# Performance work log

Hardware: AMD Instinct MI355X
Metric: run time of the kernel (lower is better)

## Reference

```python
import jax, jax.numpy as jnp
import numpy as np
from jax import lax

# quantization bit widths (config)
IB, WB, RB, AB = 8, 4, 4, 8


def quantize(x, bw):
    """Signed fixed-point quantization to bw bits in [-1, 1) with STE."""
    scale = 2.0 ** (bw - 1)
    q = jnp.clip(jnp.round(x * scale), -scale, scale - 1) / scale
    return x + lax.stop_gradient(q - x)


def setup_inputs() -> dict:
    key = jax.random.key(0)
    k1, k2, k3, k4, k5 = jax.random.split(key, 5)
    B, T, I, H, O = 256, 1024, 64, 256, 16
    inputs = jax.random.normal(k1, (B, T, I), dtype=jnp.float32)
    # input kernel init: uniform(-1, 1)
    Wi = jax.random.uniform(k2, (H, I), dtype=jnp.float32, minval=-1.0, maxval=1.0)
    # recurrent kernel: orthogonal (geotorch parametrization); materialize via QR
    A = jax.random.normal(k3, (H, H), dtype=jnp.float32)
    Wr, _ = jnp.linalg.qr(A)
    Wr = Wr.astype(jnp.float32)
    Wo = jax.random.normal(k4, (O, H), dtype=jnp.float32) * 0.1
    b = jax.random.normal(k5, (H,), dtype=jnp.float32) * 0.01
    return {"inputs": inputs, "Wi": Wi, "Wr": Wr, "Wo": Wo, "b": b}


def reference(inputs, Wi, Wr, Wo, b):
    # quantize inputs (ib bits)
    x = quantize(inputs, IB)
    # quantized input projection, precomputed for all timesteps: [B,T,H]
    u = jnp.einsum("bti,hi->bth", x, quantize(Wi, WB))
    Wrq = quantize(Wr, RB)  # quantized orthogonal recurrent weight [H,H]
    B = inputs.shape[0]
    H = Wr.shape[0]
    h0 = jnp.zeros((B, H), dtype=inputs.dtype)

    def step(h, u_t):
        z = u_t + h @ Wrq.T                      # [B,H]
        m = jax.nn.relu(jnp.abs(z) + b)          # modrelu magnitude
        h_new = quantize(jnp.sign(z) * m, AB)    # quantized activation
        return h_new, None

    u_t = jnp.swapaxes(u, 0, 1)  # [T,B,H]
    h_last, _ = lax.scan(step, h0, u_t)
    # output head on last hidden state
    out = h_last @ quantize(Wo, WB).T  # [B,O]
    return out
```

## Files before the change

### kernel.cpp

```cpp
#include <hip/hip_runtime.h>


#define TSEQ 1024
#define IDIM 64
#define HDIM 256
#define ODIM 16

__device__ __forceinline__ int sdot4i8(int a, int b, int c) {
#if __has_builtin(__builtin_amdgcn_sdot4)
    return __builtin_amdgcn_sdot4(a, b, c, false);
#else
    int r = c;
    r += ((a << 24) >> 24) * ((b << 24) >> 24);
    r += ((a << 16) >> 24) * ((b << 16) >> 24);
    r += ((a << 8)  >> 24) * ((b << 8)  >> 24);
    r += (a >> 24) * (b >> 24);
    return r;
#endif
}

__device__ __forceinline__ int qpack4(float4 f, float s, float lo, float hi) {
    int a = (int)fminf(fmaxf(rintf(f.x * s), lo), hi);
    int b = (int)fminf(fmaxf(rintf(f.y * s), lo), hi);
    int c = (int)fminf(fmaxf(rintf(f.z * s), lo), hi);
    int d = (int)fminf(fmaxf(rintf(f.w * s), lo), hi);
    return (a & 255) | ((b & 255) << 8) | ((c & 255) << 16) | ((d & 255) << 24);
}

__device__ __forceinline__ int qsum(int v) {
    v += __builtin_amdgcn_update_dpp(0, v, 0xB1, 0xF, 0xF, true);
    v += __builtin_amdgcn_update_dpp(0, v, 0x4E, 0xF, 0xF, true);
    return v;
}

__global__ __launch_bounds__(256, 1)
void qornn_kernel(const float* __restrict__ x, const float* __restrict__ Wi,
                  const float* __restrict__ Wr, const float* __restrict__ Wo,
                  const float* __restrict__ bias, float* __restrict__ out) {
    __shared__ alignas(16) int xlds[TSEQ * 16 + 16];
    __shared__ alignas(16) int wstage[8192];
    __shared__ alignas(16) int hbuf[2][64];

    const int tid = threadIdx.x;
    const int brow = blockIdx.x;
    const int w    = tid >> 6;
    const int l    = tid & 63;
    const int q    = l & 3;
    const int m16  = l >> 2;
    const int obase = w * 64 + m16 * 4;

    {
        const float4* wi4 = (const float4*)Wi;
        #pragma unroll
        for (int it = 0; it < 16; ++it) {
            int flat = it * 256 + tid;
            wstage[flat] = qpack4(wi4[flat], 8.0f, -8.0f, 7.0f);
        }
    }
    __syncthreads();
    int4 wiq[4];
    {
        const int4* p = (const int4*)wstage;
        #pragma unroll
        for (int i = 0; i < 4; ++i) wiq[i] = p[(obase + i) * 4 + q];
    }
    __syncthreads();

    int4 wr[16];
    {
        const float4* wr4 = (const float4*)Wr;
        #pragma unroll
        for (int it = 0; it < 32; ++it) {
            int flat = it * 256 + tid;
            wstage[flat] = qpack4(wr4[flat], 8.0f, -8.0f, 7.0f);
        }
        __syncthreads();
        if (obase < 128) {
            const int4* p = (const int4*)wstage;
            #pragma unroll
            for (int i = 0; i < 4; ++i)
                #pragma unroll
                for (int r = 0; r < 4; ++r)
                    wr[i * 4 + r] = p[(obase + i) * 16 + q * 4 + r];
        }
        __syncthreads();
        #pragma unroll
        for (int it = 0; it < 32; ++it) {
            int flat = it * 256 + tid;
            wstage[flat] = qpack4(wr4[8192 + flat], 8.0f, -8.0f, 7.0f);
        }
        __syncthreads();
        if (obase >= 128) {
            const int4* p = (const int4*)wstage;
            #pragma unroll
            for (int i = 0; i < 4; ++i)
                #pragma unroll
                for (int r = 0; r < 4; ++r)
                    wr[i * 4 + r] = p[(obase - 128 + i) * 16 + q * 4 + r];
        }
        __syncthreads();
    }

    {
        const float4* wo4 = (const float4*)Wo;
        #pragma unroll
        for (int it = 0; it < 4; ++it) {
            int flat = it * 256 + tid;
            wstage[flat] = qpack4(wo4[flat], 8.0f, -8.0f, 7.0f);
        }
    }

    {
        const float4* rowf4 = (const float4*)(x + (size_t)brow * (TSEQ * IDIM));
        #pragma unroll 8
        for (int it = 0; it < 64; ++it) {
            int flat = it * 256 + tid;
            xlds[flat] = qpack4(rowf4[flat], 128.0f, -128.0f, 127.0f);
        }
    }
    if (tid < 64) hbuf[0][tid] = 0;
    __syncthreads();

    const float bv = bias[tid];
    const bool qb0 = (q & 1) != 0;
    const bool qb1 = (q & 2) != 0;

    int u[4];
    {
        const int4 xx = ((const int4*)xlds)[q];
        #pragma unroll
        for (int i = 0; i < 4; ++i) {
            int s = sdot4i8(xx.x, wiq[i].x, 0);
            s = sdot4i8(xx.y, wiq[i].y, s);
            s = sdot4i8(xx.z, wiq[i].z, s);
            u[i] = sdot4i8(xx.w, wiq[i].w, s);
        }
    }

    #pragma unroll 2
    for (int t = 0; t < TSEQ; ++t) {
        int4 hh[4];
        {
            const int4* hP = (const int4*)hbuf[t & 1];
            #pragma unroll
            for (int r = 0; r < 4; ++r) hh[r] = hP[q * 4 + r];
        }
        const int4 xn = ((const int4*)xlds)[(t + 1) * 4 + q];

        int za[4], zb[4];
        #pragma unroll
        for (int i = 0; i < 4; ++i) {
            int s0 = u[i];
            s0 = sdot4i8(hh[0].x, wr[i * 4 + 0].x, s0);
            s0 = sdot4i8(hh[0].y, wr[i * 4 + 0].y, s0);
            s0 = sdot4i8(hh[0].z, wr[i * 4 + 0].z, s0);
            s0 = sdot4i8(hh[0].w, wr[i * 4 + 0].w, s0);
            s0 = sdot4i8(hh[1].x, wr[i * 4 + 1].x, s0);
            s0 = sdot4i8(hh[1].y, wr[i * 4 + 1].y, s0);
            s0 = sdot4i8(hh[1].z, wr[i * 4 + 1].z, s0);
            s0 = sdot4i8(hh[1].w, wr[i * 4 + 1].w, s0);
            int s1 = 0;
            s1 = sdot4i8(hh[2].x, wr[i * 4 + 2].x, s1);
            s1 = sdot4i8(hh[2].y, wr[i * 4 + 2].y, s1);
            s1 = sdot4i8(hh[2].z, wr[i * 4 + 2].z, s1);
            s1 = sdot4i8(hh[2].w, wr[i * 4 + 2].w, s1);
            s1 = sdot4i8(hh[3].x, wr[i * 4 + 3].x, s1);
            s1 = sdot4i8(hh[3].y, wr[i * 4 + 3].y, s1);
            s1 = sdot4i8(hh[3].z, wr[i * 4 + 3].z, s1);
            s1 = sdot4i8(hh[3].w, wr[i * 4 + 3].w, s1);
            za[i] = s0; zb[i] = s1;
        }
        int un[4];
        #pragma unroll
        for (int i = 0; i < 4; ++i) {
            int s = sdot4i8(xn.x, wiq[i].x, 0);
            s = sdot4i8(xn.y, wiq[i].y, s);
            s = sdot4i8(xn.z, wiq[i].z, s);
            un[i] = sdot4i8(xn.w, wiq[i].w, s);
        }

        const int z0 = qsum(za[0] + zb[0]);
        const int z1 = qsum(za[1] + zb[1]);
        const int z2 = qsum(za[2] + zb[2]);
        const int z3 = qsum(za[3] + zb[3]);
        const int zlo = qb0 ? z1 : z0;
        const int zhi = qb0 ? z3 : z2;
        const int z   = qb1 ? zhi : zlo;

        const float zf = (float)z;
        const float t1 = fmaf(fabsf(zf), 0.0009765625f, bv);
        const float t2 = fmaxf(t1, 0.0f);
        const float r  = rintf(t2 * 128.0f);
        const int vpos = (int)fminf(r, 127.0f);
        const int vneg = -(int)fminf(r, 128.0f);
        int hv = (z < 0) ? vneg : vpos;
        hv = (z == 0) ? 0 : hv;

        ((signed char*)hbuf[(t + 1) & 1])[tid] = (signed char)hv;

        #pragma unroll
        for (int i = 0; i < 4; ++i) u[i] = un[i];
        __syncthreads();
    }

    if (tid < ODIM) {
        const int4* wo = (const int4*)wstage;
        const int4* hl = (const int4*)hbuf[0];
        int a0 = 0, a1 = 0, a2 = 0, a3 = 0;
        #pragma unroll
        for (int i = 0; i < 16; ++i) {
            int4 w4 = wo[tid * 16 + i];
            int4 h4 = hl[i];
            a0 = sdot4i8(h4.x, w4.x, a0);
            a1 = sdot4i8(h4.y, w4.y, a1);
            a2 = sdot4i8(h4.z, w4.z, a2);
            a3 = sdot4i8(h4.w, w4.w, a3);
        }
        out[brow * ODIM + tid] = (float)((a0 + a1) + (a2 + a3)) * 0.0009765625f;
    }
}

extern "C" void kernel_launch(void* const* d_in, const int* in_sizes, int n_in,
                              void* d_out, int out_size, void* d_ws, size_t ws_size,
                              hipStream_t stream) {
    const float* x  = (const float*)d_in[0];
    const float* Wi = (const float*)d_in[1];
    const float* Wr = (const float*)d_in[2];
    const float* Wo = (const float*)d_in[3];
    const float* b  = (const float*)d_in[4];
    float* out = (float*)d_out;

    const int B = in_sizes[0] / (TSEQ * IDIM);
    qornn_kernel<<<B, HDIM, 0, stream>>>(x, Wi, Wr, Wo, b, out);
}
```

Baseline: 422.1 us.

## Compute recurrent matvec with int8 MFMA instead of per-lane sdot4 and DPP reduction

The per-step recurrent product h·Wrᵀ now runs on 16x16x64 int8 MFMA instructions, with the quantized Wr held in registers in A-operand layout and the hidden state read as the B operand. Each lane then picks its own output element out of the accumulator tile. This replaces 64 sdot4 instructions and a DPP cross-lane reduction per lane. The input projection is reorganised so each lane computes one full dot product for its output row. The B operand's 16 columns are all the same hidden vector, so most of the MFMA work is redundant. The cost being attacked is per-step instruction latency on the serial critical path.

```diff
diff --git a/kernel.cpp b/kernel.cpp
--- a/kernel.cpp
+++ b/kernel.cpp
@@ -5,6 +5,8 @@
 #define IDIM 64
 #define HDIM 256
 #define ODIM 16
+
+using i32x4 = __attribute__((ext_vector_type(4))) int;
 
 __device__ __forceinline__ int sdot4i8(int a, int b, int c) {
 #if __has_builtin(__builtin_amdgcn_sdot4)
@@ -27,12 +29,6 @@
     return (a & 255) | ((b & 255) << 8) | ((c & 255) << 16) | ((d & 255) << 24);
 }
 
-__device__ __forceinline__ int qsum(int v) {
-    v += __builtin_amdgcn_update_dpp(0, v, 0xB1, 0xF, 0xF, true);
-    v += __builtin_amdgcn_update_dpp(0, v, 0x4E, 0xF, 0xF, true);
-    return v;
-}
-
 __global__ __launch_bounds__(256, 1)
 void qornn_kernel(const float* __restrict__ x, const float* __restrict__ Wi,
                   const float* __restrict__ Wr, const float* __restrict__ Wo,
@@ -43,11 +39,12 @@
 
     const int tid = threadIdx.x;
     const int brow = blockIdx.x;
-    const int w    = tid >> 6;
-    const int l    = tid & 63;
-    const int q    = l & 3;
-    const int m16  = l >> 2;
-    const int obase = w * 64 + m16 * 4;
+    const int w   = tid >> 6;
+    const int l   = tid & 63;
+    const int lm  = l & 15;
+    const int lg  = l >> 4;
+    const int olocal = ((l & 15) >> 2) * 16 + lg * 4 + (l & 3);
+    const int oglob  = w * 64 + olocal;
 
     {
         const float4* wi4 = (const float4*)Wi;
@@ -58,15 +55,15 @@
         }
     }
     __syncthreads();
-    int4 wiq[4];
+    int4 wi[4];
     {
         const int4* p = (const int4*)wstage;
         #pragma unroll
-        for (int i = 0; i < 4; ++i) wiq[i] = p[(obase + i) * 4 + q];
+        for (int i = 0; i < 4; ++i) wi[i] = p[oglob * 4 + i];
     }
     __syncthreads();
 
-    int4 wr[16];
+    i32x4 wrA[4][4];
     {
         const float4* wr4 = (const float4*)Wr;
         #pragma unroll
@@ -75,13 +72,13 @@
             wstage[flat] = qpack4(wr4[flat], 8.0f, -8.0f, 7.0f);
         }
         __syncthreads();
-        if (obase < 128) {
-            const int4* p = (const int4*)wstage;
+        if (w < 2) {
+            const i32x4* p = (const i32x4*)wstage;
             #pragma unroll
-            for (int i = 0; i < 4; ++i)
+            for (int tt = 0; tt < 4; ++tt)
                 #pragma unroll
-                for (int r = 0; r < 4; ++r)
-                    wr[i * 4 + r] = p[(obase + i) * 16 + q * 4 + r];
+                for (int s = 0; s < 4; ++s)
+                    wrA[tt][s] = p[(w * 64 + tt * 16 + lm) * 16 + s * 4 + lg];
         }
         __syncthreads();
         #pragma unroll
@@ -90,13 +87,13 @@
             wstage[flat] = qpack4(wr4[8192 + flat], 8.0f, -8.0f, 7.0f);
         }
         __syncthreads();
-        if (obase >= 128) {
-            const int4* p = (const int4*)wstage;
+        if (w >= 2) {
+            const i32x4* p = (const i32x4*)wstage;
             #pragma unroll
-            for (int i = 0; i < 4; ++i)
+            for (int tt = 0; tt < 4; ++tt)
                 #pragma unroll
-                for (int r = 0; r < 4; ++r)
-                    wr[i * 4 + r] = p[(obase - 128 + i) * 16 + q * 4 + r];
+                for (int s = 0; s < 4; ++s)
+                    wrA[tt][s] = p[((w - 2) * 64 + tt * 16 + lm) * 16 + s * 4 + lg];
         }
         __syncthreads();
     }
@@ -121,71 +118,60 @@
     if (tid < 64) hbuf[0][tid] = 0;
     __syncthreads();
 
-    const float bv = bias[tid];
-    const bool qb0 = (q & 1) != 0;
-    const bool qb1 = (q & 2) != 0;
-
-    int u[4];
-    {
-        const int4 xx = ((const int4*)xlds)[q];
-        #pragma unroll
-        for (int i = 0; i < 4; ++i) {
-            int s = sdot4i8(xx.x, wiq[i].x, 0);
-            s = sdot4i8(xx.y, wiq[i].y, s);
-            s = sdot4i8(xx.z, wiq[i].z, s);
-            u[i] = sdot4i8(xx.w, wiq[i].w, s);
-        }
-    }
+    const float bv = bias[oglob];
+    const bool tb1 = (l & 8) != 0;
+    const bool tb0 = (l & 4) != 0;
+    const bool rb1 = (l & 2) != 0;
+    const bool rb0 = (l & 1) != 0;
+
+    int u = 0;
+    #pragma unroll
+    for (int s = 0; s < 4; ++s) {
+        const int4 xx = ((const int4*)xlds)[s];
+        u = sdot4i8(xx.x, wi[s].x, u);
+        u = sdot4i8(xx.y, wi[s].y, u);
+        u = sdot4i8(xx.z, wi[s].z, u);
+        u = sdot4i8(xx.w, wi[s].w, u);
+    }
+
+    const i32x4 zero4 = {0, 0, 0, 0};
 
     #pragma unroll 2
     for (int t = 0; t < TSEQ; ++t) {
-        int4 hh[4];
+        i32x4 hB[4];
         {
-            const int4* hP = (const int4*)hbuf[t & 1];
+            const i32x4* hP = (const i32x4*)hbuf[t & 1];
             #pragma unroll
-            for (int r = 0; r < 4; ++r) hh[r] = hP[q * 4 + r];
-        }
-        const int4 xn = ((const int4*)xlds)[(t + 1) * 4 + q];
-
-        int za[4], zb[4];
-        #pragma unroll
-        for (int i = 0; i < 4; ++i) {
-            int s0 = u[i];
-            s0 = sdot4i8(hh[0].x, wr[i * 4 + 0].x, s0);
-            s0 = sdot4i8(hh[0].y, wr[i * 4 + 0].y, s0);
-            s0 = sdot4i8(hh[0].z, wr[i * 4 + 0].z, s0);
-            s0 = sdot4i8(hh[0].w, wr[i * 4 + 0].w, s0);
-            s0 = sdot4i8(hh[1].x, wr[i * 4 + 1].x, s0);
-            s0 = sdot4i8(hh[1].y, wr[i * 4 + 1].y, s0);
-            s0 = sdot4i8(hh[1].z, wr[i * 4 + 1].z, s0);
-            s0 = sdot4i8(hh[1].w, wr[i * 4 + 1].w, s0);
-            int s1 = 0;
-            s1 = sdot4i8(hh[2].x, wr[i * 4 + 2].x, s1);
-            s1 = sdot4i8(hh[2].y, wr[i * 4 + 2].y, s1);
-            s1 = sdot4i8(hh[2].z, wr[i * 4 + 2].z, s1);
-            s1 = sdot4i8(hh[2].w, wr[i * 4 + 2].w, s1);
-            s1 = sdot4i8(hh[3].x, wr[i * 4 + 3].x, s1);
-            s1 = sdot4i8(hh[3].y, wr[i * 4 + 3].y, s1);
-            s1 = sdot4i8(hh[3].z, wr[i * 4 + 3].z, s1);
-            s1 = sdot4i8(hh[3].w, wr[i * 4 + 3].w, s1);
-            za[i] = s0; zb[i] = s1;
-        }
-        int un[4];
-        #pragma unroll
-        for (int i = 0; i < 4; ++i) {
-            int s = sdot4i8(xn.x, wiq[i].x, 0);
-            s = sdot4i8(xn.y, wiq[i].y, s);
-            s = sdot4i8(xn.z, wiq[i].z, s);
-            un[i] = sdot4i8(xn.w, wiq[i].w, s);
-        }
-
-        const int z0 = qsum(za[0] + zb[0]);
-        const int z1 = qsum(za[1] + zb[1]);
-        const int z2 = qsum(za[2] + zb[2]);
-        const int z3 = qsum(za[3] + zb[3]);
-        const int zlo = qb0 ? z1 : z0;
-        const int zhi = qb0 ? z3 : z2;
-        const int z   = qb1 ? zhi : zlo;
+            for (int s = 0; s < 4; ++s) hB[s] = hP[s * 4 + lg];
+        }
+        int4 xn[4];
+        #pragma unroll
+        for (int s = 0; s < 4; ++s) xn[s] = ((const int4*)xlds)[(t + 1) * 4 + s];
+
+        i32x4 c0 = zero4, c1 = zero4, c2 = zero4, c3 = zero4;
+        #pragma unroll
+        for (int s = 0; s < 4; ++s) {
+            c0 = __builtin_amdgcn_mfma_i32_16x16x64_i8(wrA[0][s], hB[s], c0, 0, 0, 0);
+            c1 = __builtin_amdgcn_mfma_i32_16x16x64_i8(wrA[1][s], hB[s], c1, 0, 0, 0);
+            c2 = __builtin_amdgcn_mfma_i32_16x16x64_i8(wrA[2][s], hB[s], c2, 0, 0, 0);
+            c3 = __builtin_amdgcn_mfma_i32_16x16x64_i8(wrA[3][s], hB[s], c3, 0, 0, 0);
+        }
+
+        int un = 0;
+        #pragma unroll
+        for (int s = 0; s < 4; ++s) {
+            un = sdot4i8(xn[s].x, wi[s].x, un);
+            un = sdot4i8(xn[s].y, wi[s].y, un);
+            un = sdot4i8(xn[s].z, wi[s].z, un);
+            un = sdot4i8(xn[s].w, wi[s].w, un);
+        }
+
+        const i32x4 ca = tb1 ? c2 : c0;
+        const i32x4 cb = tb1 ? c3 : c1;
+        const i32x4 ct = tb0 ? cb : ca;
+        const int zlo = rb1 ? ct[2] : ct[0];
+        const int zhi = rb1 ? ct[3] : ct[1];
+        const int z   = (rb0 ? zhi : zlo) + u;
 
         const float zf = (float)z;
         const float t1 = fmaf(fabsf(zf), 0.0009765625f, bv);
@@ -196,10 +182,9 @@
         int hv = (z < 0) ? vneg : vpos;
         hv = (z == 0) ? 0 : hv;
 
-        ((signed char*)hbuf[(t + 1) & 1])[tid] = (signed char)hv;
-
-        #pragma unroll
-        for (int i = 0; i < 4; ++i) u[i] = un[i];
+        ((signed char*)hbuf[(t + 1) & 1])[oglob] = (signed char)hv;
+
+        u = un;
         __syncthreads();
     }
 
```

Result: slower. 480.3 us (+13.8%).

## Process two batch rows per block to interleave independent recurrences

Applied to the files above, without the earlier changes.

Each block now runs the recurrence for two batch rows at once, sharing the register-resident quantized recurrent weights, and launches half as many blocks. The two independent dependency chains interleave to hide sdot4/LDS/DPP latency and halve the per-row cost of the per-step barrier. It also halves the grid (128 blocks) and needs more LDS for two x rows, with the weight staging buffer aliased onto the x buffer. On 256 CUs this leaves half the CUs idle.

```diff
diff --git a/kernel.cpp b/kernel.cpp
--- a/kernel.cpp
+++ b/kernel.cpp
@@ -5,6 +5,7 @@
 #define IDIM 64
 #define HDIM 256
 #define ODIM 16
+#define XROW (TSEQ * 16 + 16)
 
 __device__ __forceinline__ int sdot4i8(int a, int b, int c) {
 #if __has_builtin(__builtin_amdgcn_sdot4)
@@ -37,11 +38,11 @@
 void qornn_kernel(const float* __restrict__ x, const float* __restrict__ Wi,
                   const float* __restrict__ Wr, const float* __restrict__ Wo,
                   const float* __restrict__ bias, float* __restrict__ out) {
-    __shared__ alignas(16) int xlds[TSEQ * 16 + 16];
-    __shared__ alignas(16) int wstage[8192];
-    __shared__ alignas(16) int hbuf[2][64];
-
-    const int tid = threadIdx.x;
+    __shared__ alignas(16) int xlds[2][XROW];
+    __shared__ alignas(16) int wolds[1024];
+    __shared__ alignas(16) int hbuf[2][2][64];
+
+    const int tid  = threadIdx.x;
     const int brow = blockIdx.x;
     const int w    = tid >> 6;
     const int l    = tid & 63;
@@ -49,6 +50,8 @@
     const int m16  = l >> 2;
     const int obase = w * 64 + m16 * 4;
 
+    int* wstage = &xlds[0][0];
+
     {
         const float4* wi4 = (const float4*)Wi;
         #pragma unroll
@@ -106,117 +109,178 @@
         #pragma unroll
         for (int it = 0; it < 4; ++it) {
             int flat = it * 256 + tid;
-            wstage[flat] = qpack4(wo4[flat], 8.0f, -8.0f, 7.0f);
-        }
-    }
-
-    {
-        const float4* rowf4 = (const float4*)(x + (size_t)brow * (TSEQ * IDIM));
-        #pragma unroll 8
-        for (int it = 0; it < 64; ++it) {
-            int flat = it * 256 + tid;
-            xlds[flat] = qpack4(rowf4[flat], 128.0f, -128.0f, 127.0f);
-        }
-    }
-    if (tid < 64) hbuf[0][tid] = 0;
+            wolds[flat] = qpack4(wo4[flat], 8.0f, -8.0f, 7.0f);
+        }
+    }
+
+    {
+        #pragma unroll
+        for (int r = 0; r < 2; ++r) {
+            const float4* rowf4 =
+                (const float4*)(x + (size_t)(2 * brow + r) * (TSEQ * IDIM));
+            #pragma unroll 8
+            for (int it = 0; it < 64; ++it) {
+                int flat = it * 256 + tid;
+                xlds[r][flat] = qpack4(rowf4[flat], 128.0f, -128.0f, 127.0f);
+            }
+        }
+    }
+    if (tid < 128) ((int*)hbuf[0])[tid] = 0;
     __syncthreads();
 
     const float bv = bias[tid];
     const bool qb0 = (q & 1) != 0;
     const bool qb1 = (q & 2) != 0;
 
-    int u[4];
-    {
-        const int4 xx = ((const int4*)xlds)[q];
-        #pragma unroll
-        for (int i = 0; i < 4; ++i) {
-            int s = sdot4i8(xx.x, wiq[i].x, 0);
-            s = sdot4i8(xx.y, wiq[i].y, s);
-            s = sdot4i8(xx.z, wiq[i].z, s);
-            u[i] = sdot4i8(xx.w, wiq[i].w, s);
+    int uA[4], uB[4];
+    {
+        const int4 xxA = ((const int4*)xlds[0])[q];
+        const int4 xxB = ((const int4*)xlds[1])[q];
+        #pragma unroll
+        for (int i = 0; i < 4; ++i) {
+            int s = sdot4i8(xxA.x, wiq[i].x, 0);
+            s = sdot4i8(xxA.y, wiq[i].y, s);
+            s = sdot4i8(xxA.z, wiq[i].z, s);
+            uA[i] = sdot4i8(xxA.w, wiq[i].w, s);
+            int p = sdot4i8(xxB.x, wiq[i].x, 0);
+            p = sdot4i8(xxB.y, wiq[i].y, p);
+            p = sdot4i8(xxB.z, wiq[i].z, p);
+            uB[i] = sdot4i8(xxB.w, wiq[i].w, p);
         }
     }
 
     #pragma unroll 2
     for (int t = 0; t < TSEQ; ++t) {
-        int4 hh[4];
+        int4 hhA[4], hhB[4];
         {
-            const int4* hP = (const int4*)hbuf[t & 1];
-            #pragma unroll
-            for (int r = 0; r < 4; ++r) hh[r] = hP[q * 4 + r];
-        }
-        const int4 xn = ((const int4*)xlds)[(t + 1) * 4 + q];
-
-        int za[4], zb[4];
-        #pragma unroll
-        for (int i = 0; i < 4; ++i) {
-            int s0 = u[i];
-            s0 = sdot4i8(hh[0].x, wr[i * 4 + 0].x, s0);
-            s0 = sdot4i8(hh[0].y, wr[i * 4 + 0].y, s0);
-            s0 = sdot4i8(hh[0].z, wr[i * 4 + 0].z, s0);
-            s0 = sdot4i8(hh[0].w, wr[i * 4 + 0].w, s0);
-            s0 = sdot4i8(hh[1].x, wr[i * 4 + 1].x, s0);
-            s0 = sdot4i8(hh[1].y, wr[i * 4 + 1].y, s0);
-            s0 = sdot4i8(hh[1].z, wr[i * 4 + 1].z, s0);
-            s0 = sdot4i8(hh[1].w, wr[i * 4 + 1].w, s0);
+            const int4* hPA = (const int4*)hbuf[t & 1][0];
+            const int4* hPB = (const int4*)hbuf[t & 1][1];
+            #pragma unroll
+            for (int r = 0; r < 4; ++r) hhA[r] = hPA[q * 4 + r];
+            #pragma unroll
+            for (int r = 0; r < 4; ++r) hhB[r] = hPB[q * 4 + r];
+        }
+        const int4 xnA = ((const int4*)xlds[0])[(t + 1) * 4 + q];
+        const int4 xnB = ((const int4*)xlds[1])[(t + 1) * 4 + q];
+
+        int zaA[4], zbA[4], zaB[4], zbB[4];
+        #pragma unroll
+        for (int i = 0; i < 4; ++i) {
+            int s0 = uA[i];
+            s0 = sdot4i8(hhA[0].x, wr[i * 4 + 0].x, s0);
+            s0 = sdot4i8(hhA[0].y, wr[i * 4 + 0].y, s0);
+            s0 = sdot4i8(hhA[0].z, wr[i * 4 + 0].z, s0);
+            s0 = sdot4i8(hhA[0].w, wr[i * 4 + 0].w, s0);
+            s0 = sdot4i8(hhA[1].x, wr[i * 4 + 1].x, s0);
+            s0 = sdot4i8(hhA[1].y, wr[i * 4 + 1].y, s0);
+            s0 = sdot4i8(hhA[1].z, wr[i * 4 + 1].z, s0);
+            s0 = sdot4i8(hhA[1].w, wr[i * 4 + 1].w, s0);
             int s1 = 0;
-            s1 = sdot4i8(hh[2].x, wr[i * 4 + 2].x, s1);
-            s1 = sdot4i8(hh[2].y, wr[i * 4 + 2].y, s1);
-            s1 = sdot4i8(hh[2].z, wr[i * 4 + 2].z, s1);
-            s1 = sdot4i8(hh[2].w, wr[i * 4 + 2].w, s1);
-            s1 = sdot4i8(hh[3].x, wr[i * 4 + 3].x, s1);
-            s1 = sdot4i8(hh[3].y, wr[i * 4 + 3].y, s1);
-            s1 = sdot4i8(hh[3].z, wr[i * 4 + 3].z, s1);
-            s1 = sdot4i8(hh[3].w, wr[i * 4 + 3].w, s1);
-            za[i] = s0; zb[i] = s1;
-        }
-        int un[4];
-        #pragma unroll
-        for (int i = 0; i < 4; ++i) {
-            int s = sdot4i8(xn.x, wiq[i].x, 0);
-            s = sdot4i8(xn.y, wiq[i].y, s);
-            s = sdot4i8(xn.z, wiq[i].z, s);
-            un[i] = sdot4i8(xn.w, wiq[i].w, s);
-        }
-
-        const int z0 = qsum(za[0] + zb[0]);
-        const int z1 = qsum(za[1] + zb[1]);
-        const int z2 = qsum(za[2] + zb[2]);
-        const int z3 = qsum(za[3] + zb[3]);
-        const int zlo = qb0 ? z1 : z0;
-        const int zhi = qb0 ? z3 : z2;
-        const int z   = qb1 ? zhi : zlo;
-
-        const float zf = (float)z;
-        const float t1 = fmaf(fabsf(zf), 0.0009765625f, bv);
-        const float t2 = fmaxf(t1, 0.0f);
-        const float r  = rintf(t2 * 128.0f);
-        const int vpos = (int)fminf(r, 127.0f);
-        const int vneg = -(int)fminf(r, 128.0f);
-        int hv = (z < 0) ? vneg : vpos;
-        hv = (z == 0) ? 0 : hv;
-
-        ((signed char*)hbuf[(t + 1) & 1])[tid] = (signed char)hv;
-
-        #pragma unroll
-        for (int i = 0; i < 4; ++i) u[i] = un[i];
-        __syncthreads();
-    }
-
-    if (tid < ODIM) {
-        const int4* wo = (const int4*)wstage;
-        const int4* hl = (const int4*)hbuf[0];
+            s1 = sdot4i8(hhA[2].x, wr[i * 4 + 2].x, s1);
+            s1 = sdot4i8(hhA[2].y, wr[i * 4 + 2].y, s1);
+            s1 = sdot4i8(hhA[2].z, wr[i * 4 + 2].z, s1);
+            s1 = sdot4i8(hhA[2].w, wr[i * 4 + 2].w, s1);
+            s1 = sdot4i8(hhA[3].x, wr[i * 4 + 3].x, s1);
+            s1 = sdot4i8(hhA[3].y, wr[i * 4 + 3].y, s1);
+            s1 = sdot4i8(hhA[3].z, wr[i * 4 + 3].z, s1);
+            s1 = sdot4i8(hhA[3].w, wr[i * 4 + 3].w, s1);
+            zaA[i] = s0; zbA[i] = s1;
+        }
+        #pragma unroll
+        for (int i = 0; i < 4; ++i) {
+            int s0 = uB[i];
+            s0 = sdot4i8(hhB[0].x, wr[i * 4 + 0].x, s0);
+            s0 = sdot4i8(hhB[0].y, wr[i * 4 + 0].y, s0);
+            s0 = sdot4i8(hhB[0].z, wr[i * 4 + 0].z, s0);
+            s0 = sdot4i8(hhB[0].w, wr[i * 4 + 0].w, s0);
+            s0 = sdot4i8(hhB[1].x, wr[i * 4 + 1].x, s0);
+            s0 = sdot4i8(hhB[1].y, wr[i * 4 + 1].y, s0);
+            s0 = sdot4i8(hhB[1].z, wr[i * 4 + 1].z, s0);
+            s0 = sdot4i8(hhB[1].w, wr[i * 4 + 1].w, s0);
+            int s1 = 0;
+            s1 = sdot4i8(hhB[2].x, wr[i * 4 + 2].x, s1);
+            s1 = sdot4i8(hhB[2].y, wr[i * 4 + 2].y, s1);
+            s1 = sdot4i8(hhB[2].z, wr[i * 4 + 2].z, s1);
+            s1 = sdot4i8(hhB[2].w, wr[i * 4 + 2].w, s1);
+            s1 = sdot4i8(hhB[3].x, wr[i * 4 + 3].x, s1);
+            s1 = sdot4i8(hhB[3].y, wr[i * 4 + 3].y, s1);
+            s1 = sdot4i8(hhB[3].z, wr[i * 4 + 3].z, s1);
+            s1 = sdot4i8(hhB[3].w, wr[i * 4 + 3].w, s1);
+            zaB[i] = s0; zbB[i] = s1;
+        }
+
+        int unA[4], unB[4];
+        #pragma unroll
+        for (int i = 0; i < 4; ++i) {
+            int s = sdot4i8(xnA.x, wiq[i].x, 0);
+            s = sdot4i8(xnA.y, wiq[i].y, s);
+            s = sdot4i8(xnA.z, wiq[i].z, s);
+            unA[i] = sdot4i8(xnA.w, wiq[i].w, s);
+            int p = sdot4i8(xnB.x, wiq[i].x, 0);
+            p = sdot4i8(xnB.y, wiq[i].y, p);
+            p = sdot4i8(xnB.z, wiq[i].z, p);
+            unB[i] = sdot4i8(xnB.w, wiq[i].w, p);
+        }
+
+        const int z0A = qsum(zaA[0] + zbA[0]);
+        const int z1A = qsum(zaA[1] + zbA[1]);
+        const int z2A = qsum(zaA[2] + zbA[2]);
+        const int z3A = qsum(zaA[3] + zbA[3]);
+        const int z0B = qsum(zaB[0] + zbB[0]);
+        const int z1B = qsum(zaB[1] + zbB[1]);
+        const int z2B = qsum(zaB[2] + zbB[2]);
+        const int z3B = qsum(zaB[3] + zbB[3]);
+        const int zloA = qb0 ? z1A : z0A;
+        const int zhiA = qb0 ? z3A : z2A;
+        const int zA   = qb1 ? zhiA : zloA;
+        const int zloB = qb0 ? z1B : z0B;
+        const int zhiB = qb0 ? z3B : z2B;
+        const int zB   = qb1 ? zhiB : zloB;
+
+        {
+            const float zf = (float)zA;
+            const float t1 = fmaf(fabsf(zf), 0.0009765625f, bv);
+            const float t2 = fmaxf(t1, 0.0f);
+            const float r  = rintf(t2 * 128.0f);
+            const int vpos = (int)fminf(r, 127.0f);
+            const int vneg = -(int)fminf(r, 128.0f);
+            int hv = (zA < 0) ? vneg : vpos;
+            hv = (zA == 0) ? 0 : hv;
+            ((signed char*)hbuf[(t + 1) & 1][0])[tid] = (signed char)hv;
+        }
+        {
+            const float zf = (float)zB;
+            const float t1 = fmaf(fabsf(zf), 0.0009765625f, bv);
+            const float t2 = fmaxf(t1, 0.0f);
+            const float r  = rintf(t2 * 128.0f);
+            const int vpos = (int)fminf(r, 127.0f);
+            const int vneg = -(int)fminf(r, 128.0f);
+            int hv = (zB < 0) ? vneg : vpos;
+            hv = (zB == 0) ? 0 : hv;
+            ((signed char*)hbuf[(t + 1) & 1][1])[tid] = (signed char)hv;
+        }
+
+        #pragma unroll
+        for (int i = 0; i < 4; ++i) { uA[i] = unA[i]; uB[i] = unB[i]; }
+        __syncthreads();
+    }
+
+    if (tid < 2 * ODIM) {
+        const int r = tid >> 4;
+        const int o = tid & 15;
+        const int4* wo = (const int4*)wolds;
+        const int4* hl = (const int4*)hbuf[0][r];
         int a0 = 0, a1 = 0, a2 = 0, a3 = 0;
         #pragma unroll
         for (int i = 0; i < 16; ++i) {
-            int4 w4 = wo[tid * 16 + i];
+            int4 w4 = wo[o * 16 + i];
             int4 h4 = hl[i];
             a0 = sdot4i8(h4.x, w4.x, a0);
             a1 = sdot4i8(h4.y, w4.y, a1);
             a2 = sdot4i8(h4.z, w4.z, a2);
             a3 = sdot4i8(h4.w, w4.w, a3);
         }
-        out[brow * ODIM + tid] = (float)((a0 + a1) + (a2 + a3)) * 0.0009765625f;
+        out[(2 * brow + r) * ODIM + o] = (float)((a0 + a1) + (a2 + a3)) * 0.0009765625f;
     }
 }
 
@@ -231,5 +295,5 @@
     float* out = (float*)d_out;
 
     const int B = in_sizes[0] / (TSEQ * IDIM);
-    qornn_kernel<<<B, HDIM, 0, stream>>>(x, Wi, Wr, Wo, b, out);
-}
+    qornn_kernel<<<B / 2, HDIM, 0, stream>>>(x, Wi, Wr, Wo, b, out);
+}
```

After: 671.9 us. 1.59x slower.

## Compute input projection in 16-step chunks with i8 MFMA into double-buffered LDS

Applied to the files above, without the earlier changes.

Replaces the per-timestep sdot4 input projection (16 dot instructions per thread per step) with an MFMA i32_16x16x64_i8 batch computed once every 16 timesteps for the next chunk. Results go to a double-buffered LDS staging area and are read per thread each step. This takes the input-projection work off the serial recurrence path, at the cost of extra LDS, an extra LDS load per step, and a chunk-boundary MFMA burst. The x buffer is padded so the prefetch past the last step stays in bounds.

```diff
diff --git a/kernel.cpp b/kernel.cpp
--- a/kernel.cpp
+++ b/kernel.cpp
@@ -5,6 +5,10 @@
 #define IDIM 64
 #define HDIM 256
 #define ODIM 16
+#define USTRIDE 260
+#define UBUF 4160
+
+using i32x4 = __attribute__((ext_vector_type(4))) int;
 
 __device__ __forceinline__ int sdot4i8(int a, int b, int c) {
 #if __has_builtin(__builtin_amdgcn_sdot4)
@@ -37,8 +41,9 @@
 void qornn_kernel(const float* __restrict__ x, const float* __restrict__ Wi,
                   const float* __restrict__ Wr, const float* __restrict__ Wo,
                   const float* __restrict__ bias, float* __restrict__ out) {
-    __shared__ alignas(16) int xlds[TSEQ * 16 + 16];
-    __shared__ alignas(16) int wstage[8192];
+    __shared__ alignas(16) int xlds[(TSEQ + 16) * 16];
+    __shared__ alignas(16) int ustage[2 * UBUF];
+    __shared__ alignas(16) int wolds[1024];
     __shared__ alignas(16) int hbuf[2][64];
 
     const int tid = threadIdx.x;
@@ -48,21 +53,24 @@
     const int q    = l & 3;
     const int m16  = l >> 2;
     const int obase = w * 64 + m16 * 4;
+    const int lm   = l & 15;
+    const int kg   = l >> 4;
 
     {
         const float4* wi4 = (const float4*)Wi;
         #pragma unroll
         for (int it = 0; it < 16; ++it) {
             int flat = it * 256 + tid;
-            wstage[flat] = qpack4(wi4[flat], 8.0f, -8.0f, 7.0f);
-        }
-    }
-    __syncthreads();
-    int4 wiq[4];
-    {
-        const int4* p = (const int4*)wstage;
-        #pragma unroll
-        for (int i = 0; i < 4; ++i) wiq[i] = p[(obase + i) * 4 + q];
+            ustage[flat] = qpack4(wi4[flat], 8.0f, -8.0f, 7.0f);
+        }
+    }
+    __syncthreads();
+    i32x4 wiA[4];
+    {
+        const i32x4* p = (const i32x4*)ustage;
+        #pragma unroll
+        for (int tt = 0; tt < 4; ++tt)
+            wiA[tt] = p[(w * 64 + tt * 16 + lm) * 4 + kg];
     }
     __syncthreads();
 
@@ -72,11 +80,11 @@
         #pragma unroll
         for (int it = 0; it < 32; ++it) {
             int flat = it * 256 + tid;
-            wstage[flat] = qpack4(wr4[flat], 8.0f, -8.0f, 7.0f);
+            ustage[flat] = qpack4(wr4[flat], 8.0f, -8.0f, 7.0f);
         }
         __syncthreads();
         if (obase < 128) {
-            const int4* p = (const int4*)wstage;
+            const int4* p = (const int4*)ustage;
             #pragma unroll
             for (int i = 0; i < 4; ++i)
                 #pragma unroll
@@ -87,11 +95,11 @@
         #pragma unroll
         for (int it = 0; it < 32; ++it) {
             int flat = it * 256 + tid;
-            wstage[flat] = qpack4(wr4[8192 + flat], 8.0f, -8.0f, 7.0f);
+            ustage[flat] = qpack4(wr4[8192 + flat], 8.0f, -8.0f, 7.0f);
         }
         __syncthreads();
         if (obase >= 128) {
-            const int4* p = (const int4*)wstage;
+            const int4* p = (const int4*)ustage;
             #pragma unroll
             for (int i = 0; i < 4; ++i)
                 #pragma unroll
@@ -106,7 +114,7 @@
         #pragma unroll
         for (int it = 0; it < 4; ++it) {
             int flat = it * 256 + tid;
-            wstage[flat] = qpack4(wo4[flat], 8.0f, -8.0f, 7.0f);
+            wolds[flat] = qpack4(wo4[flat], 8.0f, -8.0f, 7.0f);
         }
     }
 
@@ -121,36 +129,48 @@
     if (tid < 64) hbuf[0][tid] = 0;
     __syncthreads();
 
+    {
+        const i32x4 bf = *(const i32x4*)&xlds[lm * 16 + kg * 4];
+        #pragma unroll
+        for (int tt = 0; tt < 4; ++tt) {
+            i32x4 acc = {0, 0, 0, 0};
+            acc = __builtin_amdgcn_mfma_i32_16x16x64_i8(wiA[tt], bf, acc, 0, 0, 0);
+            *(i32x4*)&ustage[lm * USTRIDE + w * 64 + tt * 16 + kg * 4] = acc;
+        }
+    }
+
     const float bv = bias[tid];
     const bool qb0 = (q & 1) != 0;
     const bool qb1 = (q & 2) != 0;
-
-    int u[4];
-    {
-        const int4 xx = ((const int4*)xlds)[q];
-        #pragma unroll
-        for (int i = 0; i < 4; ++i) {
-            int s = sdot4i8(xx.x, wiq[i].x, 0);
-            s = sdot4i8(xx.y, wiq[i].y, s);
-            s = sdot4i8(xx.z, wiq[i].z, s);
-            u[i] = sdot4i8(xx.w, wiq[i].w, s);
-        }
-    }
+    __syncthreads();
 
     #pragma unroll 2
     for (int t = 0; t < TSEQ; ++t) {
+        const int cb = (t >> 4) & 1;
+        const int ut = ustage[cb * UBUF + (t & 15) * USTRIDE + tid];
+
         int4 hh[4];
         {
             const int4* hP = (const int4*)hbuf[t & 1];
             #pragma unroll
             for (int r = 0; r < 4; ++r) hh[r] = hP[q * 4 + r];
         }
-        const int4 xn = ((const int4*)xlds)[(t + 1) * 4 + q];
+
+        if ((t & 15) == 0) {
+            const int t0 = t + 16;
+            const i32x4 bf = *(const i32x4*)&xlds[(t0 + lm) * 16 + kg * 4];
+            #pragma unroll
+            for (int tt = 0; tt < 4; ++tt) {
+                i32x4 acc = {0, 0, 0, 0};
+                acc = __builtin_amdgcn_mfma_i32_16x16x64_i8(wiA[tt], bf, acc, 0, 0, 0);
+                *(i32x4*)&ustage[(cb ^ 1) * UBUF + lm * USTRIDE + w * 64 + tt * 16 + kg * 4] = acc;
+            }
+        }
 
         int za[4], zb[4];
         #pragma unroll
         for (int i = 0; i < 4; ++i) {
-            int s0 = u[i];
+            int s0 = 0;
             s0 = sdot4i8(hh[0].x, wr[i * 4 + 0].x, s0);
             s0 = sdot4i8(hh[0].y, wr[i * 4 + 0].y, s0);
             s0 = sdot4i8(hh[0].z, wr[i * 4 + 0].z, s0);
@@ -170,14 +190,6 @@
             s1 = sdot4i8(hh[3].w, wr[i * 4 + 3].w, s1);
             za[i] = s0; zb[i] = s1;
         }
-        int un[4];
-        #pragma unroll
-        for (int i = 0; i < 4; ++i) {
-            int s = sdot4i8(xn.x, wiq[i].x, 0);
-            s = sdot4i8(xn.y, wiq[i].y, s);
-            s = sdot4i8(xn.z, wiq[i].z, s);
-            un[i] = sdot4i8(xn.w, wiq[i].w, s);
-        }
 
         const int z0 = qsum(za[0] + zb[0]);
         const int z1 = qsum(za[1] + zb[1]);
@@ -185,7 +197,7 @@
         const int z3 = qsum(za[3] + zb[3]);
         const int zlo = qb0 ? z1 : z0;
         const int zhi = qb0 ? z3 : z2;
-        const int z   = qb1 ? zhi : zlo;
+        const int z   = (qb1 ? zhi : zlo) + ut;
 
         const float zf = (float)z;
         const float t1 = fmaf(fabsf(zf), 0.0009765625f, bv);
@@ -198,13 +210,11 @@
 
         ((signed char*)hbuf[(t + 1) & 1])[tid] = (signed char)hv;
 
-        #pragma unroll
-        for (int i = 0; i < 4; ++i) u[i] = un[i];
         __syncthreads();
     }
 
     if (tid < ODIM) {
-        const int4* wo = (const int4*)wstage;
+        const int4* wo = (const int4*)wolds;
         const int4* hl = (const int4*)hbuf[0];
         int a0 = 0, a1 = 0, a2 = 0, a3 = 0;
         #pragma unroll
```

After: 421.1 us. No clear change (-0.2%).
